# Kernel optimization log

Measured on AMD Instinct MI355X. Metric: run time of the kernel, lower is better.

Reference implementation:

```python
import jax, jax.numpy as jnp
import numpy as np

B, S, D = 2, 2048, 2048
H, KV, HD = 32, 8, 64          # n_heads, n_kv_heads, head_dim
REP = H // KV                  # 4
THETA = 10000.0


def _rotate_half(u):
    h = u.shape[-1] // 2
    return jnp.concatenate([-u[..., h:], u[..., :h]], axis=-1)


def setup_inputs() -> dict:
    key = jax.random.key(0)
    ks = jax.random.split(key, 5)
    x = jax.random.normal(ks[0], (B, S, D), dtype=jnp.float32)
    Wq = jax.random.normal(ks[1], (D, H * HD), dtype=jnp.float32) * 0.02
    Wk = jax.random.normal(ks[2], (D, KV * HD), dtype=jnp.float32) * 0.02
    Wv = jax.random.normal(ks[3], (D, KV * HD), dtype=jnp.float32) * 0.02
    Wo = jax.random.normal(ks[4], (H * HD, D), dtype=jnp.float32) * 0.02
    return {"x": x, "Wq": Wq, "Wk": Wk, "Wv": Wv, "Wo": Wo}


def reference(x, Wq, Wk, Wv, Wo):
    b, s, d = x.shape
    # QKV projections (nn.Linear, no bias)
    q = (x @ Wq).reshape(b, s, H, HD).transpose(0, 2, 1, 3)   # [B,H,S,HD]
    k = (x @ Wk).reshape(b, s, KV, HD).transpose(0, 2, 1, 3)  # [B,KV,S,HD]
    v = (x @ Wv).reshape(b, s, KV, HD).transpose(0, 2, 1, 3)  # [B,KV,S,HD]

    # RoPE (position_offset = 0)
    inv_freq = 1.0 / (THETA ** (jnp.arange(0, HD, 2, dtype=jnp.float32) / HD))
    freqs = jnp.outer(jnp.arange(s, dtype=jnp.float32), inv_freq)  # [S,HD/2]
    emb = jnp.concatenate([freqs, freqs], axis=-1)                  # [S,HD]
    cos, sin = jnp.cos(emb), jnp.sin(emb)
    q = q * cos + _rotate_half(q) * sin
    k = k * cos + _rotate_half(k) * sin

    # Grouped attention: avoid materializing repeated KV tensors.
    qg = q.reshape(b, KV, REP, s, HD)                               # [B,KV,REP,S,HD]
    scale = 1.0 / np.sqrt(HD)
    scores = jnp.einsum('bgrqd,bgkd->bgrqk', qg, k) * scale         # [B,KV,REP,S,S]
    causal = jnp.tril(jnp.ones((s, s), dtype=bool))
    scores = jnp.where(causal, scores, jnp.finfo(jnp.float32).min)
    probs = jax.nn.softmax(scores.astype(jnp.float32), axis=-1).astype(q.dtype)
    out = jnp.einsum('bgrqk,bgkd->bgrqd', probs, v)                 # [B,KV,REP,S,HD]
    out = out.reshape(b, H, s, HD).transpose(0, 2, 1, 3).reshape(b, s, H * HD)
    return out @ Wo                                                  # [B,S,D]
```

## Files before the change

kernel.cpp:

```cpp
#include <hip/hip_runtime.h>
#include <math.h>

typedef __bf16 bf16_t;
typedef bf16_t bf16x8 __attribute__((ext_vector_type(8)));
typedef bf16_t bf16x4 __attribute__((ext_vector_type(4)));
typedef float floatx4 __attribute__((ext_vector_type(4)));
typedef short short4v __attribute__((ext_vector_type(4)));

#define MFMA16(a, b, c) __builtin_amdgcn_mfma_f32_16x16x32_bf16((a), (b), (c), 0, 0, 0)

#if __has_builtin(__builtin_amdgcn_exp2f)
#define PEXP(x) __builtin_amdgcn_exp2f(x)
#define SCORE_SCALE (0.125f * 1.4426950408889634f)
#else
#define PEXP(x) __expf(x)
#define SCORE_SCALE 0.125f
#endif

#if __has_builtin(__builtin_amdgcn_mfma_f32_16x16x16bf16_1k)
#define HAVE_MFMA_K16 1
__device__ __forceinline__ floatx4 mfma_k16(bf16x4 a, bf16x4 b, floatx4 c)
{
    union { bf16x4 v; short4v s; } ua, ub;
    ua.v = a; ub.v = b;
    return __builtin_amdgcn_mfma_f32_16x16x16bf16_1k(ua.s, ub.s, c, 0, 0, 0);
}
#endif

union PU { unsigned u[2]; bf16x4 v; };
union BU { unsigned u[4]; bf16x8 v; };

__device__ __forceinline__ void gld16(const void* g, void* lds)
{
    __builtin_amdgcn_global_load_lds(
        reinterpret_cast<const __attribute__((address_space(1))) void*>(
            reinterpret_cast<uintptr_t>(g)),
        reinterpret_cast<__attribute__((address_space(3))) void*>(
            (unsigned int)reinterpret_cast<uintptr_t>(lds)),
        16, 0, 0);
}

template <int N>
__device__ __forceinline__ void vmw()
{
    __asm__ volatile("s_waitcnt vmcnt(%0)" :: "n"(N) : "memory");
}

__device__ __forceinline__ void barx()
{
    __asm__ volatile("" ::: "memory");
    __builtin_amdgcn_s_barrier();
    __asm__ volatile("" ::: "memory");
}

__device__ __forceinline__ void lgk0()
{
    __asm__ volatile("s_waitcnt lgkmcnt(0)" ::: "memory");
}

__device__ __forceinline__ void stage128(
    const bf16_t* __restrict__ g, int K, int r0, int k0,
    bf16_t* lds, int tid, int wave)
{
    #pragma unroll
    for (int i = 0; i < 4; ++i) {
        int c = i * 256 + tid, r = c >> 3, s = c & 7;
        gld16(g + (size_t)(r0 + r) * K + k0 + ((s ^ (r & 7)) << 3),
              lds + (size_t)(i * 256 + wave * 64) * 8);
    }
}

template <typename TC>
__device__ __forceinline__ void gemm128_body(
    const bf16_t* __restrict__ A, const bf16_t* __restrict__ Bt,
    TC* __restrict__ C, int row0, int col0, int N, int K, bf16_t* smem)
{
    const int tid  = threadIdx.x;
    const int wave = tid >> 6, lane = tid & 63;
    const int quad = lane >> 4, l16 = lane & 15;
    const int wm = (wave >> 1) * 64;
    const int wn = (wave & 1) * 64;

    bf16_t* As0 = smem;
    bf16_t* As1 = smem + 8192;
    bf16_t* Bs0 = smem + 16384;
    bf16_t* Bs1 = smem + 24576;

    const int ntile = K >> 6;

    floatx4 acc[4][4] = {};

    stage128(A, K, row0, 0, As0, tid, wave);
    stage128(Bt, K, col0, 0, Bs0, tid, wave);

    #pragma unroll 1
    for (int u = 0; u < ntile; ++u) {
        const int d = u & 1;
        bf16_t* Asd = d ? As1 : As0;
        bf16_t* Bsd = d ? Bs1 : Bs0;

        if (u + 1 < ntile) {
            stage128(A, K, row0, (u + 1) << 6, d ? As0 : As1, tid, wave);
            stage128(Bt, K, col0, (u + 1) << 6, d ? Bs0 : Bs1, tid, wave);
            vmw<8>();
        } else {
            vmw<0>();
        }
        barx();

        bf16x8 af[4][2], bfr[4][2];
        #pragma unroll
        for (int mt = 0; mt < 4; ++mt)
            #pragma unroll
            for (int kh = 0; kh < 2; ++kh) {
                int ar = wm + mt * 16 + l16;
                af[mt][kh] = *(const bf16x8*)&Asd[ar * 64 +
                    (((kh * 4 + quad) ^ (ar & 7)) << 3)];
            }
        #pragma unroll
        for (int nt = 0; nt < 4; ++nt)
            #pragma unroll
            for (int kh = 0; kh < 2; ++kh) {
                int br = wn + nt * 16 + l16;
                bfr[nt][kh] = *(const bf16x8*)&Bsd[br * 64 +
                    (((kh * 4 + quad) ^ (br & 7)) << 3)];
            }

        __builtin_amdgcn_s_setprio(1);
        #pragma unroll
        for (int kh = 0; kh < 2; ++kh)
            #pragma unroll
            for (int mt = 0; mt < 4; ++mt)
                #pragma unroll
                for (int nt = 0; nt < 4; ++nt)
                    acc[mt][nt] = MFMA16(af[mt][kh], bfr[nt][kh], acc[mt][nt]);
        __builtin_amdgcn_s_setprio(0);

        lgk0();
        barx();
    }

    #pragma unroll
    for (int mt = 0; mt < 4; ++mt)
        #pragma unroll
        for (int nt = 0; nt < 4; ++nt)
            #pragma unroll
            for (int r = 0; r < 4; ++r)
                C[(size_t)(row0 + wm + mt * 16 + quad * 4 + r) * N
                  + col0 + wn + nt * 16 + l16] = (TC)acc[mt][nt][r];
}

__global__ __launch_bounds__(256, 2) void gemm128_qkv(
    const bf16_t* __restrict__ A, const bf16_t* __restrict__ BtQ,
    const bf16_t* __restrict__ BtK, const bf16_t* __restrict__ BtV,
    bf16_t* __restrict__ CQ, bf16_t* __restrict__ CK, bf16_t* __restrict__ CV)
{
    extern __shared__ __align__(16) bf16_t smem[];
    const int bid = blockIdx.x;
    const int l = (bid & 7) * 96 + (bid >> 3);
    const int x = l % 24;
    const int y = l / 24;
    const bf16_t* Bt; bf16_t* C; int N, col0;
    if (x < 16)      { Bt = BtQ; C = CQ; N = 2048; col0 = x * 128; }
    else if (x < 20) { Bt = BtK; C = CK; N = 512;  col0 = (x - 16) * 128; }
    else             { Bt = BtV; C = CV; N = 512;  col0 = (x - 20) * 128; }
    gemm128_body<bf16_t>(A, Bt, C, y * 128, col0, N, 2048, smem);
}

__global__ __launch_bounds__(256, 2) void gemm128_out(
    const bf16_t* __restrict__ A, const bf16_t* __restrict__ Bt,
    float* __restrict__ C)
{
    extern __shared__ __align__(16) bf16_t smem[];
    const int bid = blockIdx.x;
    const int l = (bid & 7) * 64 + (bid >> 3);
    const int x = l & 15;
    const int y = l >> 4;
    gemm128_body<float>(A, Bt, C, y * 128, x * 128, 2048, 2048, smem);
}

__device__ __forceinline__ void transpose_body(
    const float* __restrict__ W, bf16_t* __restrict__ Wt, int K, int N,
    int bx, int by, float (*t)[33], int tid)
{
    int tx = tid & 31, ty = tid >> 5;
    #pragma unroll
    for (int i = 0; i < 32; i += 8)
        t[ty + i][tx] = W[(size_t)(by + ty + i) * N + bx + tx];
    __syncthreads();
    #pragma unroll
    for (int i = 0; i < 32; i += 8)
        Wt[(size_t)(bx + ty + i) * K + by + tx] = (bf16_t)t[tx][ty + i];
}

__global__ __launch_bounds__(256) void prep_all(
    const float* __restrict__ x, const float* __restrict__ Wq,
    const float* __restrict__ Wk, const float* __restrict__ Wv,
    bf16_t* __restrict__ xb, bf16_t* __restrict__ WqT,
    bf16_t* __restrict__ WkT, bf16_t* __restrict__ WvT)
{
    __shared__ float t[32][33];
    const int blk = blockIdx.x, tid = threadIdx.x;
    if (blk < 8192) {
        int i = blk * 256 + tid;
        float4 f = ((const float4*)x)[i];
        bf16x4 v = {(bf16_t)f.x, (bf16_t)f.y, (bf16_t)f.z, (bf16_t)f.w};
        ((bf16x4*)xb)[i] = v;
    } else if (blk < 12288) {
        int r = blk - 8192;
        transpose_body(Wq, WqT, 2048, 2048, (r & 63) * 32, (r >> 6) * 32, t, tid);
    } else if (blk < 13312) {
        int r = blk - 12288;
        transpose_body(Wk, WkT, 2048, 512, (r & 15) * 32, (r >> 4) * 32, t, tid);
    } else {
        int r = blk - 13312;
        transpose_body(Wv, WvT, 2048, 512, (r & 15) * 32, (r >> 4) * 32, t, tid);
    }
}

__global__ __launch_bounds__(256) void mid_all(
    bf16_t* __restrict__ Kw, const bf16_t* __restrict__ Vw,
    bf16_t* __restrict__ VtG, const float* __restrict__ Wo,
    bf16_t* __restrict__ WoT)
{
    __shared__ float tf[32][33];
    __shared__ bf16_t tb[32][34];
    const int blk = blockIdx.x, tid = threadIdx.x;
    if (blk < 4096) {
        int idx = blk * 256 + tid;
        int i   = idx & 31;
        int h   = (idx >> 5) & 7;
        int row = idx >> 8;
        int pos = row & 2047;
        float invf = powf(10000.0f, -(float)i / 32.0f);
        float sv, cv;
        sincosf((float)pos * invf, &sv, &cv);
        size_t base = (size_t)row * 512 + (size_t)h * 64 + i;
        float a  = (float)Kw[base];
        float b2 = (float)Kw[base + 32];
        Kw[base]      = (bf16_t)(a * cv - b2 * sv);
        Kw[base + 32] = (bf16_t)(b2 * cv + a * sv);
    } else if (blk < 6144) {
        int r  = blk - 4096;
        int bz = r >> 10, r2 = r & 1023;
        int bx = (r2 & 15) * 32, by = (r2 >> 4) * 32;
        int tx = tid & 31, ty = tid >> 5;
        #pragma unroll
        for (int i = 0; i < 32; i += 8)
            tb[ty + i][tx] = Vw[((size_t)bz * 2048 + by + ty + i) * 512 + bx + tx];
        __syncthreads();
        #pragma unroll
        for (int i = 0; i < 32; i += 8)
            VtG[((size_t)bz * 512 + bx + ty + i) * 2048 + by + tx] = tb[tx][ty + i];
    } else {
        int r = blk - 6144;
        transpose_body(Wo, WoT, 2048, 2048, (r & 63) * 32, (r >> 6) * 32, tf, tid);
    }
}

__global__ __launch_bounds__(256, 2) void gqa_attn(
    const bf16_t* __restrict__ Q, const bf16_t* __restrict__ Kc,
    const bf16_t* __restrict__ Vt, bf16_t* __restrict__ AO)
{
    __shared__ alignas(16) bf16_t Ks[2][128 * 64];
    __shared__ alignas(16) bf16_t Vs[2][128 * 64];

    const int bid = blockIdx.x;
    const int l   = (bid & 7) * 64 + (bid >> 3);
    const int g   = l >> 6;
    const int b   = (l >> 5) & 1;
    const int x   = l & 31;

    const int tid  = threadIdx.x;
    const int wave = tid >> 6, lane = tid & 63;
    const int quad = lane >> 4, l16 = lane & 15;
    const int h = g * 4 + wave;

    #pragma unroll 1
    for (int t = 0; t < 2; ++t) {
        const int qt = t ? x : (63 - x);
        const int q0 = qt * 32;
        int qb[2];
        qb[0] = q0;
        qb[1] = q0 + 16;

        bf16x8 qf[2][2];
        #pragma unroll
        for (int mt = 0; mt < 2; ++mt) {
            int qrow = qb[mt] + l16;
            const bf16_t* qp = Q + (size_t)(b * 2048 + qrow) * 2048 + h * 64 + quad * 8;
            bf16x8 lo = *(const bf16x8*)qp;
            bf16x8 hi = *(const bf16x8*)(qp + 32);
            #pragma unroll
            for (int j = 0; j < 8; ++j) {
                int d = quad * 8 + j;
                float invf = powf(10000.0f, -(float)d / 32.0f);
                float sv, cv;
                sincosf((float)qrow * invf, &sv, &cv);
                float a = (float)lo[j], c2 = (float)hi[j];
                qf[mt][0][j] = (bf16_t)((a * cv - c2 * sv) * SCORE_SCALE);
                qf[mt][1][j] = (bf16_t)((c2 * cv + a * sv) * SCORE_SCALE);
            }
        }

        floatx4 o[2][4] = {};
        floatx4 ls4[2] = {};

        const int ktmax = qt >> 1;
        const int nwin  = (ktmax >> 1) + 1;

        auto STAGE = [&](int win, int dst) {
            const int kbase = win * 128;
            #pragma unroll
            for (int i = 0; i < 4; ++i) {
                int c = i * 256 + tid, r = c >> 3, s = c & 7;
                int sw = (s ^ (r & 7)) << 3;
                gld16(Kc + (size_t)(b * 2048 + kbase + r) * 512 + g * 64 + sw,
                      &Ks[dst][(i * 256 + wave * 64) * 8]);
            }
            #pragma unroll
            for (int i = 0; i < 4; ++i) {
                int c = i * 256 + tid;
                int ci = c & 511, hw = c >> 9;
                int r = ci >> 3, s = ci & 7;
                int sw = (s ^ (r & 7)) << 3;
                gld16(Vt + (size_t)(b * 512 + g * 64 + r) * 2048
                         + kbase + hw * 64 + sw,
                      &Vs[dst][(i * 256 + wave * 64) * 8]);
            }
        };

        __asm__ volatile("s_waitcnt lgkmcnt(0)" ::: "memory");
        __builtin_amdgcn_s_barrier();
        STAGE(0, 0);

        #pragma unroll 1
        for (int win = 0; win < nwin; ++win) {
            const int cur = win & 1;
            if (win + 1 < nwin) {
                STAGE(win + 1, cur ^ 1);
                __asm__ volatile("s_waitcnt vmcnt(8)" ::: "memory");
            } else {
                __asm__ volatile("s_waitcnt vmcnt(0)" ::: "memory");
            }
            __builtin_amdgcn_s_barrier();

            #pragma unroll
            for (int hw = 0; hw < 2; ++hw) {
                const int kt = 2 * win + hw;
                if (kt <= ktmax) {
                    const bf16_t* Ksh = &Ks[cur][hw * 4096];
                    const bf16_t* Vsh = &Vs[cur][hw * 4096];

                    floatx4 st[2][4] = {};
                    __builtin_amdgcn_s_setprio(1);
                    #pragma unroll
                    for (int nt = 0; nt < 4; ++nt) {
                        int kr = nt * 16 + l16;
                        bf16x8 kf0 = *(const bf16x8*)&Ksh[kr * 64 + ((quad ^ (kr & 7)) << 3)];
                        bf16x8 kf1 = *(const bf16x8*)&Ksh[kr * 64 + (((4 + quad) ^ (kr & 7)) << 3)];
                        st[0][nt] = MFMA16(kf0, qf[0][0], st[0][nt]);
                        st[0][nt] = MFMA16(kf1, qf[0][1], st[0][nt]);
                        st[1][nt] = MFMA16(kf0, qf[1][0], st[1][nt]);
                        st[1][nt] = MFMA16(kf1, qf[1][1], st[1][nt]);
                    }
                    __builtin_amdgcn_s_setprio(0);

                    PU pk[2][4];
                    const bool diag = (kt == ktmax);
                    #pragma unroll
                    for (int mt = 0; mt < 2; ++mt) {
                        const int qa = qb[mt] + l16;
                        #pragma unroll
                        for (int nt = 0; nt < 4; ++nt) {
                            float pv[4];
                            #pragma unroll
                            for (int r = 0; r < 4; ++r) {
                                float e = PEXP(st[mt][nt][r]);
                                if (diag) {
                                    int ka = kt * 64 + nt * 16 + quad * 4 + r;
                                    if (ka > qa) e = 0.f;
                                }
                                ls4[mt][r] += e;
                                pv[r] = e;
                            }
                            pk[mt][nt].v = bf16x4{(bf16_t)pv[0], (bf16_t)pv[1],
                                                  (bf16_t)pv[2], (bf16_t)pv[3]};
                        }
                    }

#ifdef HAVE_MFMA_K16
                    __builtin_amdgcn_s_setprio(1);
                    #pragma unroll
                    for (int nt = 0; nt < 4; ++nt)
                        #pragma unroll
                        for (int dt = 0; dt < 4; ++dt) {
                            int vr = dt * 16 + l16;
                            int slot = ((nt << 1) | (quad >> 1)) ^ (vr & 7);
                            bf16x4 va = *(const bf16x4*)&Vsh[vr * 64 + (slot << 3)
                                                             + ((quad & 1) << 2)];
                            o[0][dt] = mfma_k16(va, pk[0][nt].v, o[0][dt]);
                            o[1][dt] = mfma_k16(va, pk[1][nt].v, o[1][dt]);
                        }
                    __builtin_amdgcn_s_setprio(0);
#else
                    #pragma unroll
                    for (int H = 0; H < 2; ++H) {
                        BU bfv[2];
                        #pragma unroll
                        for (int mt = 0; mt < 2; ++mt) {
                            #pragma unroll
                            for (int j = 0; j < 4; ++j) {
                                int srcl = (((quad & 1) << 1) + (j >> 1)) * 16 + l16;
                                unsigned a0 = (unsigned)__shfl((int)pk[mt][2 * H].u[j & 1], srcl, 64);
                                unsigned a1 = (unsigned)__shfl((int)pk[mt][2 * H + 1].u[j & 1], srcl, 64);
                                bfv[mt].u[j] = (quad >> 1) ? a1 : a0;
                            }
                        }
                        #pragma unroll
                        for (int dt = 0; dt < 4; ++dt) {
                            int vr = dt * 16 + l16;
                            bf16x8 va = *(const bf16x8*)&Vsh[vr * 64
                                          + ((((H << 2) | quad) ^ (vr & 7)) << 3)];
                            o[0][dt] = MFMA16(va, bfv[0].v, o[0][dt]);
                            o[1][dt] = MFMA16(va, bfv[1].v, o[1][dt]);
                        }
                    }
#endif
                }
            }

            __asm__ volatile("s_waitcnt lgkmcnt(0)" ::: "memory");
            __builtin_amdgcn_s_barrier();
        }

        #pragma unroll
        for (int mt = 0; mt < 2; ++mt) {
            float l2 = ls4[mt][0] + ls4[mt][1] + ls4[mt][2] + ls4[mt][3];
            l2 += __shfl_xor(l2, 16, 64);
            l2 += __shfl_xor(l2, 32, 64);
            float rc = 1.0f / l2;
            #pragma unroll
            for (int dt = 0; dt < 4; ++dt) {
                bf16x4 ov = {(bf16_t)(o[mt][dt][0] * rc), (bf16_t)(o[mt][dt][1] * rc),
                             (bf16_t)(o[mt][dt][2] * rc), (bf16_t)(o[mt][dt][3] * rc)};
                *(bf16x4*)&AO[(size_t)(b * 2048 + qb[mt] + l16) * 2048
                              + h * 64 + dt * 16 + quad * 4] = ov;
            }
        }
    }
}

extern "C" void kernel_launch(void* const* d_in, const int* in_sizes, int n_in,
                              void* d_out, int out_size, void* d_ws, size_t ws_size,
                              hipStream_t stream)
{
    const float* x  = (const float*)d_in[0];
    const float* Wq = (const float*)d_in[1];
    const float* Wk = (const float*)d_in[2];
    const float* Wv = (const float*)d_in[3];
    const float* Wo = (const float*)d_in[4];
    float* out = (float*)d_out;

    const size_t MB = 1024 * 1024;
    char* ws = (char*)d_ws;
    bf16_t* xb_AO = (bf16_t*)(ws);
    bf16_t* WqoT  = (bf16_t*)(ws + 16 * MB);
    bf16_t* WkT   = (bf16_t*)(ws + 24 * MB);
    bf16_t* WvT   = (bf16_t*)(ws + 26 * MB);
    bf16_t* Qw    = (bf16_t*)(ws + 28 * MB);
    bf16_t* Kw    = (bf16_t*)(ws + 44 * MB);
    bf16_t* Vw    = (bf16_t*)(ws + 48 * MB);
    bf16_t* VtG   = (bf16_t*)(ws + 52 * MB);

    static bool s_attr = false;
    if (!s_attr) {
        hipFuncSetAttribute(reinterpret_cast<const void*>(gemm128_qkv),
                            hipFuncAttributeMaxDynamicSharedMemorySize, 65536);
        hipFuncSetAttribute(reinterpret_cast<const void*>(gemm128_out),
                            hipFuncAttributeMaxDynamicSharedMemorySize, 65536);
        s_attr = true;
    }

    prep_all<<<14336, 256, 0, stream>>>(x, Wq, Wk, Wv, xb_AO, WqoT, WkT, WvT);

    gemm128_qkv<<<dim3(768), 256, 65536, stream>>>(
        xb_AO, WqoT, WkT, WvT, Qw, Kw, Vw);

    mid_all<<<10240, 256, 0, stream>>>(Kw, Vw, VtG, Wo, WqoT);

    gqa_attn<<<dim3(512), 256, 0, stream>>>(Qw, Kw, VtG, xb_AO);

    gemm128_out<<<dim3(512), 256, 65536, stream>>>(xb_AO, WqoT, out);
}
```

Baseline: 274.7 us.

## Replace double-buffered GEMM pipeline with single-buffered static LDS tiles

The two 128x128 GEMM kernels drop their double-buffered LDS prefetch pipeline and custom waitcnt/barrier helpers. Each k-tile is now loaded into one static 32KB LDS buffer between two __syncthreads. Launch bounds rise from 2 to 3 blocks per CU, and the dynamic shared memory setup is removed. The aim is more resident blocks for latency hiding, at the cost of no overlap between global loads and MFMA inside a block plus an extra barrier per tile.

```diff
diff --git a/kernel.cpp b/kernel.cpp
--- a/kernel.cpp
+++ b/kernel.cpp
@@ -40,24 +40,6 @@
         16, 0, 0);
 }
 
-template <int N>
-__device__ __forceinline__ void vmw()
-{
-    __asm__ volatile("s_waitcnt vmcnt(%0)" :: "n"(N) : "memory");
-}
-
-__device__ __forceinline__ void barx()
-{
-    __asm__ volatile("" ::: "memory");
-    __builtin_amdgcn_s_barrier();
-    __asm__ volatile("" ::: "memory");
-}
-
-__device__ __forceinline__ void lgk0()
-{
-    __asm__ volatile("s_waitcnt lgkmcnt(0)" ::: "memory");
-}
-
 __device__ __forceinline__ void stage128(
     const bf16_t* __restrict__ g, int K, int r0, int k0,
     bf16_t* lds, int tid, int wave)
@@ -73,7 +55,8 @@
 template <typename TC>
 __device__ __forceinline__ void gemm128_body(
     const bf16_t* __restrict__ A, const bf16_t* __restrict__ Bt,
-    TC* __restrict__ C, int row0, int col0, int N, int K, bf16_t* smem)
+    TC* __restrict__ C, int row0, int col0, int N, int K,
+    bf16_t* As, bf16_t* Bs)
 {
     const int tid  = threadIdx.x;
     const int wave = tid >> 6, lane = tid & 63;
@@ -81,32 +64,16 @@
     const int wm = (wave >> 1) * 64;
     const int wn = (wave & 1) * 64;
 
-    bf16_t* As0 = smem;
-    bf16_t* As1 = smem + 8192;
-    bf16_t* Bs0 = smem + 16384;
-    bf16_t* Bs1 = smem + 24576;
-
     const int ntile = K >> 6;
 
     floatx4 acc[4][4] = {};
-
-    stage128(A, K, row0, 0, As0, tid, wave);
-    stage128(Bt, K, col0, 0, Bs0, tid, wave);
 
     #pragma unroll 1
     for (int u = 0; u < ntile; ++u) {
-        const int d = u & 1;
-        bf16_t* Asd = d ? As1 : As0;
-        bf16_t* Bsd = d ? Bs1 : Bs0;
-
-        if (u + 1 < ntile) {
-            stage128(A, K, row0, (u + 1) << 6, d ? As0 : As1, tid, wave);
-            stage128(Bt, K, col0, (u + 1) << 6, d ? Bs0 : Bs1, tid, wave);
-            vmw<8>();
-        } else {
-            vmw<0>();
-        }
-        barx();
+        __syncthreads();
+        stage128(A, K, row0, u << 6, As, tid, wave);
+        stage128(Bt, K, col0, u << 6, Bs, tid, wave);
+        __syncthreads();
 
         bf16x8 af[4][2], bfr[4][2];
         #pragma unroll
@@ -114,7 +81,7 @@
             #pragma unroll
             for (int kh = 0; kh < 2; ++kh) {
                 int ar = wm + mt * 16 + l16;
-                af[mt][kh] = *(const bf16x8*)&Asd[ar * 64 +
+                af[mt][kh] = *(const bf16x8*)&As[ar * 64 +
                     (((kh * 4 + quad) ^ (ar & 7)) << 3)];
             }
         #pragma unroll
@@ -122,7 +89,7 @@
             #pragma unroll
             for (int kh = 0; kh < 2; ++kh) {
                 int br = wn + nt * 16 + l16;
-                bfr[nt][kh] = *(const bf16x8*)&Bsd[br * 64 +
+                bfr[nt][kh] = *(const bf16x8*)&Bs[br * 64 +
                     (((kh * 4 + quad) ^ (br & 7)) << 3)];
             }
 
@@ -135,9 +102,6 @@
                 for (int nt = 0; nt < 4; ++nt)
                     acc[mt][nt] = MFMA16(af[mt][kh], bfr[nt][kh], acc[mt][nt]);
         __builtin_amdgcn_s_setprio(0);
-
-        lgk0();
-        barx();
     }
 
     #pragma unroll
@@ -150,12 +114,13 @@
                   + col0 + wn + nt * 16 + l16] = (TC)acc[mt][nt][r];
 }
 
-__global__ __launch_bounds__(256, 2) void gemm128_qkv(
+__global__ __launch_bounds__(256, 3) void gemm128_qkv(
     const bf16_t* __restrict__ A, const bf16_t* __restrict__ BtQ,
     const bf16_t* __restrict__ BtK, const bf16_t* __restrict__ BtV,
     bf16_t* __restrict__ CQ, bf16_t* __restrict__ CK, bf16_t* __restrict__ CV)
 {
-    extern __shared__ __align__(16) bf16_t smem[];
+    __shared__ alignas(16) bf16_t As[128 * 64];
+    __shared__ alignas(16) bf16_t Bs[128 * 64];
     const int bid = blockIdx.x;
     const int l = (bid & 7) * 96 + (bid >> 3);
     const int x = l % 24;
@@ -164,19 +129,20 @@
     if (x < 16)      { Bt = BtQ; C = CQ; N = 2048; col0 = x * 128; }
     else if (x < 20) { Bt = BtK; C = CK; N = 512;  col0 = (x - 16) * 128; }
     else             { Bt = BtV; C = CV; N = 512;  col0 = (x - 20) * 128; }
-    gemm128_body<bf16_t>(A, Bt, C, y * 128, col0, N, 2048, smem);
-}
-
-__global__ __launch_bounds__(256, 2) void gemm128_out(
+    gemm128_body<bf16_t>(A, Bt, C, y * 128, col0, N, 2048, As, Bs);
+}
+
+__global__ __launch_bounds__(256, 3) void gemm128_out(
     const bf16_t* __restrict__ A, const bf16_t* __restrict__ Bt,
     float* __restrict__ C)
 {
-    extern __shared__ __align__(16) bf16_t smem[];
+    __shared__ alignas(16) bf16_t As[128 * 64];
+    __shared__ alignas(16) bf16_t Bs[128 * 64];
     const int bid = blockIdx.x;
     const int l = (bid & 7) * 64 + (bid >> 3);
     const int x = l & 15;
     const int y = l >> 4;
-    gemm128_body<float>(A, Bt, C, y * 128, x * 128, 2048, 2048, smem);
+    gemm128_body<float>(A, Bt, C, y * 128, x * 128, 2048, 2048, As, Bs);
 }
 
 __device__ __forceinline__ void transpose_body(
@@ -473,23 +439,14 @@
     bf16_t* Vw    = (bf16_t*)(ws + 48 * MB);
     bf16_t* VtG   = (bf16_t*)(ws + 52 * MB);
 
-    static bool s_attr = false;
-    if (!s_attr) {
-        hipFuncSetAttribute(reinterpret_cast<const void*>(gemm128_qkv),
-                            hipFuncAttributeMaxDynamicSharedMemorySize, 65536);
-        hipFuncSetAttribute(reinterpret_cast<const void*>(gemm128_out),
-                            hipFuncAttributeMaxDynamicSharedMemorySize, 65536);
-        s_attr = true;
-    }
-
     prep_all<<<14336, 256, 0, stream>>>(x, Wq, Wk, Wv, xb_AO, WqoT, WkT, WvT);
 
-    gemm128_qkv<<<dim3(768), 256, 65536, stream>>>(
+    gemm128_qkv<<<dim3(768), 256, 0, stream>>>(
         xb_AO, WqoT, WkT, WvT, Qw, Kw, Vw);
 
     mid_all<<<10240, 256, 0, stream>>>(Kw, Vw, VtG, Wo, WqoT);
 
     gqa_attn<<<dim3(512), 256, 0, stream>>>(Qw, Kw, VtG, xb_AO);
 
-    gemm128_out<<<dim3(512), 256, 65536, stream>>>(xb_AO, WqoT, out);
-}
+    gemm128_out<<<dim3(512), 256, 0, stream>>>(xb_AO, WqoT, out);
+}
```

Result: no change. 275.1 us (+0.1%).
